# Performance work log

Hardware: AMD Instinct MI355X
Metric: run time of the kernel (lower is better)

The kernel has to match this reference:

```python
import jax, jax.numpy as jnp
import numpy as np

E, B, C = 4, 262144, 128  # edge types, tokens, feature dim

def setup_inputs() -> dict:
    key = jax.random.key(0)
    k1, k2, k3 = jax.random.split(key, 3)
    xs = jax.random.normal(k1, (E, B, C), dtype=jnp.float32)
    Ws = jax.random.normal(k2, (E, C, C), dtype=jnp.float32) * (1.0 / np.sqrt(C))
    bs = jax.random.normal(k3, (E, C), dtype=jnp.float32) * 0.01
    return {"xs": xs, "Ws": Ws, "bs": bs}

def reference(xs, Ws, bs):
    # Per-edge-type op: y_e = xs[e] @ Ws[e] + bs[e]  (Linear per from_node type)
    # Aggregation: sum over edges.
    # Fused grouped form: contract over edge axis e and input channel c in one einsum.
    out = jnp.einsum('ebc,ecd->bd', xs, Ws)          # [B, C]
    out = out + bs.sum(axis=0)                       # bias from each edge op, summed by aggregation
    return out
```

## Files before the change

kernel.cpp:

```cpp
#include <hip/hip_runtime.h>
#include <hip/hip_bf16.h>

#define N_E 4
#define N_B 262144
#define N_C 128

typedef __attribute__((ext_vector_type(8))) short bf16x8;
typedef __attribute__((ext_vector_type(4))) float f32x4;
typedef __attribute__((ext_vector_type(4))) unsigned int u32x4;

__device__ __forceinline__ unsigned pk2(float lo, float hi) {
  float2 t; t.x = lo; t.y = hi;
  __hip_bfloat162 h = __float22bfloat162_rn(t);
  union { __hip_bfloat162 h; unsigned u; } c;
  c.h = h;
  return c.u;
}

__global__ void __launch_bounds__(1024, 4)
grouped_gemm(const float* __restrict__ xs, const float* __restrict__ Ws,
             const float* __restrict__ bs, float* __restrict__ out) {
  extern __shared__ unsigned char smem[];
  unsigned short* lds_w = (unsigned short*)smem;

  const int tid  = threadIdx.x;
  const int lane = tid & 63;
  const int wave = tid >> 6;
  const int l15  = lane & 15;
  const int hi   = lane >> 4;
  const int waveRow = blockIdx.x * 256 + wave * 16;

  float bias[8];
#pragma unroll
  for (int n = 0; n < 8; ++n) {
    int d = n * 16 + l15;
    bias[n] = bs[d] + bs[128 + d] + bs[256 + d] + bs[384 + d];
  }

#pragma unroll
  for (int i = 0; i < 8; ++i) {
    int m = tid + i * 1024;
    int e = m >> 11;
    int u = (m >> 7) & 15;
    int d = m & 127;
    const float* src = Ws + e * (N_C * N_C) + u * 8 * N_C + d;
    float v[8];
#pragma unroll
    for (int j = 0; j < 8; ++j) v[j] = src[j * N_C];
    u32x4 pk;
#pragma unroll
    for (int j = 0; j < 4; ++j) pk[j] = pk2(v[2 * j], v[2 * j + 1]);
    *reinterpret_cast<u32x4*>(&lds_w[(size_t)m * 8]) = pk;
  }

  asm volatile("s_waitcnt vmcnt(0)" ::: "memory");
  __syncthreads();

  const unsigned vb = (unsigned)(waveRow + l15) * 512u + (unsigned)hi * 32u;
  const unsigned long long xbase = (unsigned long long)xs;

  f32x4 A0[4], A1[4];

#define AISSUE(c)                                                              \
  do {                                                                         \
    unsigned o;                                                                \
    asm volatile("v_add_u32 %0, %1, %2"                                        \
                 : "=v"(o)                                                     \
                 : "n"(((c) >> 2) * 134217728u + ((c) & 3) * 128u), "v"(vb));  \
    asm volatile("global_load_dwordx4 %0, %2, %3 offset:0\n\t"                 \
                 "global_load_dwordx4 %1, %2, %3 offset:16"                    \
                 : "=&v"(A0[(c) & 3]), "=&v"(A1[(c) & 3])                      \
                 : "v"(o), "s"(xbase)                                          \
                 : "memory");                                                  \
  } while (0)

#define WAITV(n)                                  \
  do {                                            \
    asm volatile("s_waitcnt vmcnt(" #n ")" ::: "memory"); \
    __builtin_amdgcn_sched_barrier(0);            \
  } while (0)

  f32x4 acc[8];
#pragma unroll
  for (int n = 0; n < 8; ++n) {
    f32x4 z = {0.0f, 0.0f, 0.0f, 0.0f};
    acc[n] = z;
  }

  AISSUE(0); AISSUE(1); AISSUE(2); AISSUE(3);

#define STEP(s, w)                                                             \
  do {                                                                         \
    WAITV(w);                                                                  \
    f32x4 a0 = A0[(s) & 3];                                                    \
    f32x4 a1 = A1[(s) & 3];                                                    \
    bf16x8 afrag;                                                              \
    unsigned* au = reinterpret_cast<unsigned*>(&afrag);                        \
    au[0] = pk2(a0[0], a0[1]);                                                 \
    au[1] = pk2(a0[2], a0[3]);                                                 \
    au[2] = pk2(a1[0], a1[1]);                                                 \
    au[3] = pk2(a1[2], a1[3]);                                                 \
    if ((s) <= 11) AISSUE((s) + 4);                                            \
    const unsigned short* wb =                                                 \
        lds_w + (size_t)((((s) >> 2) * 16 + ((s) & 3) * 4 + hi) * 128 + l15) * 8; \
    _Pragma("unroll")                                                          \
    for (int n = 0; n < 8; ++n) {                                              \
      bf16x8 bfrag = *reinterpret_cast<const bf16x8*>(wb + (size_t)n * 128);   \
      acc[n] = __builtin_amdgcn_mfma_f32_16x16x32_bf16(afrag, bfrag, acc[n], 0, 0, 0); \
    }                                                                          \
  } while (0)

  STEP(0, 6);  STEP(1, 6);  STEP(2, 6);  STEP(3, 6);
  STEP(4, 6);  STEP(5, 6);  STEP(6, 6);  STEP(7, 6);
  STEP(8, 6);  STEP(9, 6);  STEP(10, 6); STEP(11, 6);
  STEP(12, 6); STEP(13, 4); STEP(14, 2); STEP(15, 0);

#undef STEP
#undef WAITV
#undef AISSUE

#pragma unroll
  for (int n = 0; n < 8; ++n) {
    int d = n * 16 + l15;
#pragma unroll
    for (int r = 0; r < 4; ++r) {
      int row = waveRow + hi * 4 + r;
      out[(size_t)row * N_C + d] = acc[n][r] + bias[n];
    }
  }
}

extern "C" void kernel_launch(void* const* d_in, const int* in_sizes, int n_in,
                              void* d_out, int out_size, void* d_ws, size_t ws_size,
                              hipStream_t stream) {
  const float* xs = (const float*)d_in[0];
  const float* Ws = (const float*)d_in[1];
  const float* bs = (const float*)d_in[2];
  float* out = (float*)d_out;

  const size_t smem = 131072;
  hipFuncSetAttribute((const void*)grouped_gemm,
                      hipFuncAttributeMaxDynamicSharedMemorySize, (int)smem);

  dim3 grid(N_B / 256);
  dim3 block(1024);
  hipLaunchKernelGGL(grouped_gemm, grid, block, smem, stream, xs, Ws, bs, out);
}
```

Baseline: 145.9 us.

## Process four row tiles per block to amortize weight staging, vectorize stores

Each block now covers 1024 rows in four 256-row tiles, so the bf16 weight conversion into LDS is paid once per four tiles instead of once per tile. The load pipeline runs continuously across tile boundaries. MFMA operands are swapped so each lane holds four contiguous output columns, letting the epilogue write float4 stores with bias read from LDS. The trade-off is a grid four times smaller (256 blocks), which may underfill the GPU, plus a longer serial chain per block.

```diff
diff --git a/kernel.cpp b/kernel.cpp
--- a/kernel.cpp
+++ b/kernel.cpp
@@ -21,21 +21,15 @@
 grouped_gemm(const float* __restrict__ xs, const float* __restrict__ Ws,
              const float* __restrict__ bs, float* __restrict__ out) {
   extern __shared__ unsigned char smem[];
-  unsigned short* lds_w = (unsigned short*)smem;
+  unsigned short* lds_w   = (unsigned short*)smem;
+  float*          lds_bias = (float*)(smem + 131072);
 
   const int tid  = threadIdx.x;
   const int lane = tid & 63;
   const int wave = tid >> 6;
   const int l15  = lane & 15;
   const int hi   = lane >> 4;
-  const int waveRow = blockIdx.x * 256 + wave * 16;
-
-  float bias[8];
-#pragma unroll
-  for (int n = 0; n < 8; ++n) {
-    int d = n * 16 + l15;
-    bias[n] = bs[d] + bs[128 + d] + bs[256 + d] + bs[384 + d];
-  }
+  const int rowBase = blockIdx.x * 1024 + wave * 16;
 
 #pragma unroll
   for (int i = 0; i < 8; ++i) {
@@ -52,11 +46,13 @@
     for (int j = 0; j < 4; ++j) pk[j] = pk2(v[2 * j], v[2 * j + 1]);
     *reinterpret_cast<u32x4*>(&lds_w[(size_t)m * 8]) = pk;
   }
-
+  if (tid < 128) {
+    lds_bias[tid] = bs[tid] + bs[128 + tid] + bs[256 + tid] + bs[384 + tid];
+  }
   asm volatile("s_waitcnt vmcnt(0)" ::: "memory");
   __syncthreads();
 
-  const unsigned vb = (unsigned)(waveRow + l15) * 512u + (unsigned)hi * 32u;
+  const unsigned vb = (unsigned)(rowBase + l15) * 512u + (unsigned)hi * 32u;
   const unsigned long long xbase = (unsigned long long)xs;
 
   f32x4 A0[4], A1[4];
@@ -66,7 +62,9 @@
     unsigned o;                                                                \
     asm volatile("v_add_u32 %0, %1, %2"                                        \
                  : "=v"(o)                                                     \
-                 : "n"(((c) >> 2) * 134217728u + ((c) & 3) * 128u), "v"(vb));  \
+                 : "n"((((c) >> 4) * 131072u) + ((((c) >> 2) & 3) * 134217728u) \
+                       + (((c) & 3) * 128u)),                                  \
+                   "v"(vb));                                                   \
     asm volatile("global_load_dwordx4 %0, %2, %3 offset:0\n\t"                 \
                  "global_load_dwordx4 %1, %2, %3 offset:16"                    \
                  : "=&v"(A0[(c) & 3]), "=&v"(A1[(c) & 3])                      \
@@ -74,10 +72,10 @@
                  : "memory");                                                  \
   } while (0)
 
-#define WAITV(n)                                  \
-  do {                                            \
+#define WAITV(n)                                          \
+  do {                                                    \
     asm volatile("s_waitcnt vmcnt(" #n ")" ::: "memory"); \
-    __builtin_amdgcn_sched_barrier(0);            \
+    __builtin_amdgcn_sched_barrier(0);                    \
   } while (0)
 
   f32x4 acc[8];
@@ -89,45 +87,65 @@
 
   AISSUE(0); AISSUE(1); AISSUE(2); AISSUE(3);
 
-#define STEP(s, w)                                                             \
+#define STEP(t, w)                                                             \
   do {                                                                         \
     WAITV(w);                                                                  \
-    f32x4 a0 = A0[(s) & 3];                                                    \
-    f32x4 a1 = A1[(s) & 3];                                                    \
-    bf16x8 afrag;                                                              \
-    unsigned* au = reinterpret_cast<unsigned*>(&afrag);                        \
+    f32x4 a0 = A0[(t) & 3];                                                    \
+    f32x4 a1 = A1[(t) & 3];                                                    \
+    bf16x8 xfrag;                                                              \
+    unsigned* au = reinterpret_cast<unsigned*>(&xfrag);                        \
     au[0] = pk2(a0[0], a0[1]);                                                 \
     au[1] = pk2(a0[2], a0[3]);                                                 \
     au[2] = pk2(a1[0], a1[1]);                                                 \
     au[3] = pk2(a1[2], a1[3]);                                                 \
-    if ((s) <= 11) AISSUE((s) + 4);                                            \
+    if ((t) <= 59) AISSUE((t) + 4);                                            \
     const unsigned short* wb =                                                 \
-        lds_w + (size_t)((((s) >> 2) * 16 + ((s) & 3) * 4 + hi) * 128 + l15) * 8; \
+        lds_w + (size_t)(((((t) >> 2) & 3) * 16 + ((t) & 3) * 4 + hi) * 128 + l15) * 8; \
     _Pragma("unroll")                                                          \
     for (int n = 0; n < 8; ++n) {                                              \
-      bf16x8 bfrag = *reinterpret_cast<const bf16x8*>(wb + (size_t)n * 128);   \
-      acc[n] = __builtin_amdgcn_mfma_f32_16x16x32_bf16(afrag, bfrag, acc[n], 0, 0, 0); \
+      bf16x8 wfrag = *reinterpret_cast<const bf16x8*>(wb + (size_t)n * 128);   \
+      acc[n] = __builtin_amdgcn_mfma_f32_16x16x32_bf16(wfrag, xfrag, acc[n], 0, 0, 0); \
+    }                                                                          \
+  } while (0)
+
+#define EPILOGUE(rt)                                                           \
+  do {                                                                         \
+    float* ob = out + (size_t)(rowBase + (rt) * 256 + l15) * N_C + hi * 4;     \
+    _Pragma("unroll")                                                          \
+    for (int n = 0; n < 8; ++n) {                                              \
+      f32x4 bv = *reinterpret_cast<const f32x4*>(&lds_bias[n * 16 + hi * 4]);  \
+      f32x4 v = acc[n] + bv;                                                   \
+      *reinterpret_cast<f32x4*>(ob + n * 16) = v;                              \
+      f32x4 z = {0.0f, 0.0f, 0.0f, 0.0f};                                      \
+      acc[n] = z;                                                              \
     }                                                                          \
   } while (0)
 
   STEP(0, 6);  STEP(1, 6);  STEP(2, 6);  STEP(3, 6);
   STEP(4, 6);  STEP(5, 6);  STEP(6, 6);  STEP(7, 6);
   STEP(8, 6);  STEP(9, 6);  STEP(10, 6); STEP(11, 6);
-  STEP(12, 6); STEP(13, 4); STEP(14, 2); STEP(15, 0);
+  STEP(12, 6); STEP(13, 6); STEP(14, 6); STEP(15, 6);
+  EPILOGUE(0);
+  STEP(16, 14); STEP(17, 14); STEP(18, 14); STEP(19, 14);
+  STEP(20, 6);  STEP(21, 6);  STEP(22, 6);  STEP(23, 6);
+  STEP(24, 6);  STEP(25, 6);  STEP(26, 6);  STEP(27, 6);
+  STEP(28, 6);  STEP(29, 6);  STEP(30, 6);  STEP(31, 6);
+  EPILOGUE(1);
+  STEP(32, 14); STEP(33, 14); STEP(34, 14); STEP(35, 14);
+  STEP(36, 6);  STEP(37, 6);  STEP(38, 6);  STEP(39, 6);
+  STEP(40, 6);  STEP(41, 6);  STEP(42, 6);  STEP(43, 6);
+  STEP(44, 6);  STEP(45, 6);  STEP(46, 6);  STEP(47, 6);
+  EPILOGUE(2);
+  STEP(48, 14); STEP(49, 14); STEP(50, 14); STEP(51, 14);
+  STEP(52, 6);  STEP(53, 6);  STEP(54, 6);  STEP(55, 6);
+  STEP(56, 6);  STEP(57, 6);  STEP(58, 6);  STEP(59, 6);
+  STEP(60, 6);  STEP(61, 4);  STEP(62, 2);  STEP(63, 0);
+  EPILOGUE(3);
 
 #undef STEP
+#undef EPILOGUE
 #undef WAITV
 #undef AISSUE
-
-#pragma unroll
-  for (int n = 0; n < 8; ++n) {
-    int d = n * 16 + l15;
-#pragma unroll
-    for (int r = 0; r < 4; ++r) {
-      int row = waveRow + hi * 4 + r;
-      out[(size_t)row * N_C + d] = acc[n][r] + bias[n];
-    }
-  }
 }
 
 extern "C" void kernel_launch(void* const* d_in, const int* in_sizes, int n_in,
@@ -138,11 +156,11 @@
   const float* bs = (const float*)d_in[2];
   float* out = (float*)d_out;
 
-  const size_t smem = 131072;
+  const size_t smem = 131072 + 512;
   hipFuncSetAttribute((const void*)grouped_gemm,
                       hipFuncAttributeMaxDynamicSharedMemorySize, (int)smem);
 
-  dim3 grid(N_B / 256);
+  dim3 grid(N_B / 1024);
   dim3 block(1024);
   hipLaunchKernelGGL(grouped_gemm, grid, block, smem, stream, xs, Ws, bs, out);
 }
```

Result: slower. 152.0 us (+4.2%).
